# Kernel optimization log

Measured on AMD Instinct MI355X. Metric: run time of the kernel, lower is better.

The kernel has to match this reference:

```python
import jax, jax.numpy as jnp
import numpy as np

# Static config (matches init_kwargs)
B = 1; Z = 64; H = 64; W = 64; C = 96
NH = 3; WS = 4; SS = 2
N = WS ** 3                      # tokens per 3D window = 64
NW = (Z // WS) * (H // WS) * (W // WS)   # num windows = 4096
SCALE = (C // NH) ** -0.5
EPS = 1e-5


def _rel_pos_index():
    # same construction as WindowAttention3D.__init__ (torch.meshgrid default 'ij')
    coords = np.stack(np.meshgrid(np.arange(WS), np.arange(WS), np.arange(WS), indexing='ij'))
    cf = coords.reshape(3, -1)                       # (3, N)
    rc = (cf[:, :, None] - cf[:, None, :]).transpose(1, 2, 0)  # (N, N, 3)
    rc[:, :, 0] += WS - 1; rc[:, :, 1] += WS - 1; rc[:, :, 2] += WS - 1
    rc[:, :, 0] *= (2 * WS - 1) ** 2
    rc[:, :, 1] *= (2 * WS - 1)
    return rc.sum(-1)                                # (N, N) int


def _attn_mask():
    # shifted-window mask, as in SwinTransformerBlock3D.__init__
    img = np.zeros((Z, H, W), dtype=np.float32)
    sl = (slice(0, -WS), slice(-WS, -SS), slice(-SS, None))
    cnt = 0
    for z in sl:
        for h in sl:
            for w in sl:
                img[z, h, w] = cnt
                cnt += 1
    mw = img.reshape(Z // WS, WS, H // WS, WS, W // WS, WS)
    mw = mw.transpose(0, 2, 4, 1, 3, 5).reshape(-1, N)        # (nW, N)
    am = mw[:, None, :] - mw[:, :, None]                      # (nW, N, N)
    return np.where(am != 0, np.float32(-100.0), np.float32(0.0))


REL_IDX = jnp.asarray(_rel_pos_index())        # (N, N) int32, closed-over constant
ATTN_MASK = jnp.asarray(_attn_mask())          # (nW, N, N) float32


def _layernorm(x, g, b):
    m = x.mean(-1, keepdims=True)
    v = ((x - m) ** 2).mean(-1, keepdims=True)
    return (x - m) * jax.lax.rsqrt(v + EPS) * g + b


def _window_partition(x):
    # (B, Z, H, W, C) -> (B*nW, N, C)
    x = x.reshape(B, Z // WS, WS, H // WS, WS, W // WS, WS, C)
    return x.transpose(0, 1, 3, 5, 2, 4, 6, 7).reshape(-1, N, C)


def _window_reverse(wins):
    # (B*nW, N, C) -> (B, Z, H, W, C)
    x = wins.reshape(B, Z // WS, H // WS, W // WS, WS, WS, WS, C)
    return x.transpose(0, 1, 4, 2, 5, 3, 6, 7).reshape(B, Z, H, W, C)


def setup_inputs() -> dict:
    key = jax.random.key(0)
    ks = jax.random.split(key, 8)
    d = {
        'x': jax.random.normal(ks[0], (B, Z * H * W, C), jnp.float32),
        'norm1_w': jnp.ones((C,), jnp.float32),
        'norm1_b': jnp.zeros((C,), jnp.float32),
        'qkv_w': jax.random.normal(ks[1], (3 * C, C), jnp.float32) * 0.02,
        'qkv_b': jnp.zeros((3 * C,), jnp.float32),
        'rel_bias': jax.random.normal(ks[2], ((2 * WS - 1) ** 3, NH), jnp.float32) * 0.02,
        'proj_w': jax.random.normal(ks[3], (C, C), jnp.float32) * 0.02,
        'proj_b': jnp.zeros((C,), jnp.float32),
        'norm2_w': jnp.ones((C,), jnp.float32),
        'norm2_b': jnp.zeros((C,), jnp.float32),
        'fc1_w': jax.random.normal(ks[4], (4 * C, C), jnp.float32) * 0.02,
        'fc1_b': jnp.zeros((4 * C,), jnp.float32),
        'fc2_w': jax.random.normal(ks[5], (C, 4 * C), jnp.float32) * 0.02,
        'fc2_b': jnp.zeros((C,), jnp.float32),
    }
    return d


def reference(x, norm1_w, norm1_b, qkv_w, qkv_b, rel_bias, proj_w, proj_b,
              norm2_w, norm2_b, fc1_w, fc1_b, fc2_w, fc2_b):
    shortcut = x
    h = _layernorm(x, norm1_w, norm1_b).reshape(B, Z, H, W, C)
    # cyclic shift (SW-MSA)
    h = jnp.roll(h, (-SS, -SS, -SS), axis=(1, 2, 3))
    xw = _window_partition(h)                                  # (B*nW, N, C)
    qkv = (xw @ qkv_w.T + qkv_b).reshape(-1, N, 3, NH, C // NH)
    qkv = qkv.transpose(2, 0, 3, 1, 4)                         # (3, B_, NH, N, hd)
    q, k, v = qkv[0] * SCALE, qkv[1], qkv[2]
    attn = jnp.einsum('bhnd,bhmd->bhnm', q, k)                 # (B_, NH, N, N)
    bias = rel_bias[REL_IDX.reshape(-1)].reshape(N, N, NH).transpose(2, 0, 1)
    attn = attn + bias[None]
    attn = attn.reshape(B, NW, NH, N, N) + ATTN_MASK[None, :, None]
    attn = jax.nn.softmax(attn.reshape(-1, NH, N, N), axis=-1)
    out = jnp.einsum('bhnm,bhmd->bhnd', attn, v)
    out = out.transpose(0, 2, 1, 3).reshape(-1, N, C)
    out = out @ proj_w.T + proj_b
    h = _window_reverse(out)
    h = jnp.roll(h, (SS, SS, SS), axis=(1, 2, 3)).reshape(B, Z * H * W, C)
    x = shortcut + h                                            # residual (drop_path=0)
    y = _layernorm(x, norm2_w, norm2_b)
    y = jax.nn.gelu(y @ fc1_w.T + fc1_b, approximate=False)
    y = y @ fc2_w.T + fc2_b
    return x + y
```

## Files before the change

kernel.cpp:

```cpp
#include <hip/hip_runtime.h>

typedef __attribute__((ext_vector_type(8))) short short8;
typedef __attribute__((ext_vector_type(4))) float f32x4;

static __device__ __forceinline__ unsigned short f2bf(float f) {
  return (unsigned short)((__builtin_bit_cast(unsigned int, f) + 0x8000u) >> 16);
}
static __device__ __forceinline__ float bf2f(unsigned short u) {
  return __builtin_bit_cast(float, ((unsigned)u) << 16);
}
static __device__ __forceinline__ unsigned cvtpk(float a, float b) {
  unsigned r;
  asm("v_cvt_pk_bf16_f32 %0, %1, %2" : "=v"(r) : "v"(a), "v"(b));
  return r;
}

constexpr float LOG2E = 1.4426950408889634f;
constexpr float QSCL = 0.17677669529663687f * LOG2E;
constexpr int XP = 104;
constexpr int KP = 104;
constexpr int VTP = 72;

static __device__ __forceinline__ int frag_src(int o, int K) {
  const int j = o & 7;
  const int lane = (o >> 3) & 63;
  const int f = o >> 9;
  const int nks = K >> 5;
  const int ks = f % nks;
  const int t = f / nks;
  const int row = t * 16 + (lane & 15);
  const int k = ks * 32 + (lane >> 4) * 8 + j;
  return row * K + k;
}

__global__ void prep_kernel(const float* __restrict__ qkvw, const float* __restrict__ projw,
                            const float* __restrict__ fc1w, const float* __restrict__ fc2w,
                            const float* __restrict__ relbias,
                            unsigned short* __restrict__ ws, float* __restrict__ tab) {
  int i = blockIdx.x * 256 + threadIdx.x;
  if (i < 27648) ws[i] = f2bf(qkvw[frag_src(i, 96)] * (i < 9216 ? QSCL : 1.f));
  if (i < 9216)  ws[27648 + i] = f2bf(projw[frag_src(i, 96)]);
  if (i < 36864) {
    ws[36864 + i] = f2bf(fc1w[frag_src(i, 96)]);
    ws[73728 + i] = f2bf(fc2w[frag_src(i, 384)]);
  }
  if (i < 98304) {
    const int r = i & 3, kgi = (i >> 2) & 3, q = (i >> 4) & 63, nt = (i >> 10) & 3;
    const int vh = i >> 12;
    const int h = vh % 3, v = vh / 3;
    const int key = nt * 16 + kgi * 4 + r;
    const bool bz = v & 4, bh = v & 2, bw = v & 1;
    const int iz = q >> 4, ih = (q >> 2) & 3, iw = q & 3;
    const int jz = key >> 4, jh = (key >> 2) & 3, jw = key & 3;
    const int idx = (iz - jz + 3) * 49 + (ih - jh + 3) * 7 + (iw - jw + 3);
    const int ci = (bz ? (iz < 2 ? 9 : 18) : 0) + (bh ? (ih < 2 ? 3 : 6) : 0) +
                   (bw ? (iw < 2 ? 1 : 2) : 0);
    const int cj = (bz ? (jz < 2 ? 9 : 18) : 0) + (bh ? (jh < 2 ? 3 : 6) : 0) +
                   (bw ? (jw < 2 ? 1 : 2) : 0);
    tab[i] = (relbias[idx * 3 + h] + (ci != cj ? -100.f : 0.f)) * LOG2E;
  }
}

__global__ __launch_bounds__(256, 4) void fused_kernel(
    const float* __restrict__ x,
    const float* __restrict__ n1w, const float* __restrict__ n1b,
    const float* __restrict__ qkvb, const float* __restrict__ tab,
    const float* __restrict__ projb,
    const float* __restrict__ n2w, const float* __restrict__ n2b,
    const float* __restrict__ b1, const float* __restrict__ b2,
    const unsigned short* __restrict__ wq, const unsigned short* __restrict__ wp,
    const unsigned short* __restrict__ w1, const unsigned short* __restrict__ w2,
    float* __restrict__ out) {
  __shared__ unsigned short Xo[64 * XP];
  __shared__ unsigned short Kb[64 * KP];
  __shared__ unsigned short Vt[96 * VTP];

  const int tid = threadIdx.x;
  const int bid = blockIdx.x;
  const int wz = bid >> 8, wh = (bid >> 4) & 15, ww = bid & 15;
  const int wave = tid >> 6, lane = tid & 63;
  const int ln = lane & 15, kg = lane >> 4;

  {
    const int n = tid >> 2, part = tid & 3;
    const int lz = n >> 4, lh = (n >> 2) & 3, lw = n & 3;
    const int sz = (wz * 4 + lz + 2) & 63;
    const int sh = (wh * 4 + lh + 2) & 63;
    const int sw = (ww * 4 + lw + 2) & 63;
    const float* px = x + (size_t)((sz * 64 + sh) * 64 + sw) * 96 + part * 24;
    float4 v[6];
#pragma unroll
    for (int j = 0; j < 6; ++j) v[j] = ((const float4*)px)[j];
    float s = 0.f, sq = 0.f;
#pragma unroll
    for (int j = 0; j < 6; ++j) {
      s += v[j].x + v[j].y + v[j].z + v[j].w;
      sq += v[j].x * v[j].x + v[j].y * v[j].y + v[j].z * v[j].z + v[j].w * v[j].w;
    }
    s += __shfl_xor(s, 1);  s += __shfl_xor(s, 2);
    sq += __shfl_xor(sq, 1); sq += __shfl_xor(sq, 2);
    const float mean = s * (1.f / 96.f);
    const float var = sq * (1.f / 96.f) - mean * mean;
    const float rs = rsqrtf(var + 1e-5f);
    const float4* g4 = (const float4*)(n1w + part * 24);
    const float4* b4 = (const float4*)(n1b + part * 24);
#pragma unroll
    for (int j = 0; j < 6; ++j) {
      float4 g = g4[j], b = b4[j];
      uint2 o;
      o.x = cvtpk((v[j].x - mean) * rs * g.x + b.x, (v[j].y - mean) * rs * g.y + b.y);
      o.y = cvtpk((v[j].z - mean) * rs * g.z + b.z, (v[j].w - mean) * rs * g.w + b.w);
      *(uint2*)&Xo[n * XP + part * 24 + j * 4] = o;
    }
  }

  short8 qa[3];
  {
    short8 a[3];
#pragma unroll
    for (int ks = 0; ks < 3; ++ks)
      a[ks] = *(const short8*)&Xo[(wave * 16 + ln) * XP + ks * 32 + kg * 8];
#pragma unroll
    for (int g = 0; g < 3; ++g) {
      short8 wf[6];
#pragma unroll
      for (int f = 0; f < 6; ++f)
        wf[f] = *(const short8*)&wq[(size_t)(g * 6 + f) * 512 + lane * 8];
#pragma unroll
      for (int t = 0; t < 2; ++t) {
        const int nt = g * 2 + t;
        const int oc = nt * 16 + ln;
        f32x4 acc = {0.f, 0.f, 0.f, 0.f};
#pragma unroll
        for (int ks = 0; ks < 3; ++ks)
          acc = __builtin_amdgcn_mfma_f32_16x16x32_bf16(a[ks], wf[t * 3 + ks], acc, 0, 0, 0);
        const float bias = qkvb[oc];
#pragma unroll
        for (int r = 0; r < 4; ++r)
          Kb[(wave * 16 + kg * 4 + r) * KP + oc] = f2bf(fmaf(bias, QSCL, acc[r]));
      }
    }
#pragma unroll
    for (int h = 0; h < 3; ++h)
      qa[h] = *(const short8*)&Kb[(wave * 16 + ln) * KP + h * 32 + kg * 8];
  }
  __syncthreads();

  {
    const int t0 = wave < 2 ? 6 + 2 * wave : 8 + wave;
    const int t1 = wave < 2 ? 7 + 2 * wave : 10 + 2 * wave;
    const int t2 = wave < 2 ? 12 + wave : 11 + 2 * wave;
#pragma unroll
    for (int i = 0; i < 3; ++i) {
      const int tile = i == 0 ? t0 : (i == 1 ? t1 : t2);
      const int oc = tile * 16 + ln;
      short8 wf[3];
#pragma unroll
      for (int ks = 0; ks < 3; ++ks)
        wf[ks] = *(const short8*)&wq[(size_t)(tile * 3 + ks) * 512 + lane * 8];
      const float bias = qkvb[oc];
#pragma unroll
      for (int rt = 0; rt < 4; ++rt) {
        f32x4 acc = {0.f, 0.f, 0.f, 0.f};
#pragma unroll
        for (int ks = 0; ks < 3; ++ks) {
          short8 a = *(const short8*)&Xo[(rt * 16 + ln) * XP + ks * 32 + kg * 8];
          acc = __builtin_amdgcn_mfma_f32_16x16x32_bf16(a, wf[ks], acc, 0, 0, 0);
        }
        if (tile < 12) {
#pragma unroll
          for (int r = 0; r < 4; ++r)
            Kb[(rt * 16 + kg * 4 + r) * KP + (tile - 12 + 6) * 16 + ln] = f2bf(acc[r] + bias);
        } else {
          uint2 u;
          u.x = cvtpk(acc[0] + bias, acc[1] + bias);
          u.y = cvtpk(acc[2] + bias, acc[3] + bias);
          *(uint2*)&Vt[((tile - 12) * 16 + ln) * VTP + rt * 16 + kg * 4] = u;
        }
      }
    }
  }
  __syncthreads();

  const int vv = ((wz == 15) ? 4 : 0) | ((wh == 15) ? 2 : 0) | ((ww == 15) ? 1 : 0);
  const float* tb0 = tab + (size_t)(vv * 3) * 4096;
  const int rowbase = wave * 16 + kg * 4;
  const int lA = ((kg & 1) << 5) + ln;
  const int lB = lA + 16;
#pragma unroll
  for (int h = 0; h < 3; ++h) {
    const float* tb = tb0 + h * 4096;
    f32x4 e[4];
#pragma unroll
    for (int nt = 0; nt < 4; ++nt) {
      short8 kf = *(const short8*)&Kb[(nt * 16 + ln) * KP + h * 32 + kg * 8];
      f32x4 trow = *(const f32x4*)(tb + nt * 1024 + (wave * 16 + ln) * 16 + kg * 4);
      f32x4 z = {0.f, 0.f, 0.f, 0.f};
      f32x4 st = __builtin_amdgcn_mfma_f32_16x16x32_bf16(kf, qa[h], z, 0, 0, 0);
#pragma unroll
      for (int r = 0; r < 4; ++r)
        e[nt][r] = __builtin_amdgcn_exp2f(st[r] + trow[r]);
    }
    float hs = 0.f;
#pragma unroll
    for (int nt = 0; nt < 4; ++nt)
#pragma unroll
      for (int r = 0; r < 4; ++r) hs += e[nt][r];
    hs += __shfl_xor(hs, 16);
    hs += __shfl_xor(hs, 32);
    const float inv = __builtin_amdgcn_rcpf(hs);
    unsigned pp[4][2];
#pragma unroll
    for (int nt = 0; nt < 4; ++nt) {
      pp[nt][0] = cvtpk(e[nt][0] * inv, e[nt][1] * inv);
      pp[nt][1] = cvtpk(e[nt][2] * inv, e[nt][3] * inv);
    }
    short8 paf[2];
#pragma unroll
    for (int ks = 0; ks < 2; ++ks) {
      const unsigned a0 = __shfl((int)pp[2 * ks][0], lA);
      const unsigned a1 = __shfl((int)pp[2 * ks][1], lA);
      const unsigned a2 = __shfl((int)pp[2 * ks][0], lB);
      const unsigned a3 = __shfl((int)pp[2 * ks][1], lB);
      const unsigned b0 = __shfl((int)pp[2 * ks + 1][0], lA);
      const unsigned b1 = __shfl((int)pp[2 * ks + 1][1], lA);
      const unsigned b2 = __shfl((int)pp[2 * ks + 1][0], lB);
      const unsigned b3 = __shfl((int)pp[2 * ks + 1][1], lB);
      const bool hi = (kg >> 1) != 0;
      uint4 wv;
      wv.x = hi ? b0 : a0;
      wv.y = hi ? b1 : a1;
      wv.z = hi ? b2 : a2;
      wv.w = hi ? b3 : a3;
      paf[ks] = __builtin_bit_cast(short8, wv);
    }
#pragma unroll
    for (int dt = 0; dt < 2; ++dt) {
      f32x4 oacc = {0.f, 0.f, 0.f, 0.f};
#pragma unroll
      for (int ks = 0; ks < 2; ++ks) {
        short8 vb = *(const short8*)&Vt[(h * 32 + dt * 16 + ln) * VTP + ks * 32 + kg * 8];
        oacc = __builtin_amdgcn_mfma_f32_16x16x32_bf16(paf[ks], vb, oacc, 0, 0, 0);
      }
#pragma unroll
      for (int r = 0; r < 4; ++r)
        Xo[(rowbase + r) * XP + h * 32 + dt * 16 + ln] = f2bf(oacc[r]);
    }
  }
  __syncthreads();

  unsigned short* X2b = Vt;

  {
    int gtok[4];
#pragma unroll
    for (int r = 0; r < 4; ++r) {
      const int n = rowbase + r;
      const int lz = n >> 4, lh = (n >> 2) & 3, lw = n & 3;
      const int oz = (wz * 4 + lz + 2) & 63;
      const int oh = (wh * 4 + lh + 2) & 63;
      const int ow = (ww * 4 + lw + 2) & 63;
      gtok[r] = (oz * 64 + oh) * 64 + ow;
    }
    short8 oa[3];
#pragma unroll
    for (int ks = 0; ks < 3; ++ks)
      oa[ks] = *(const short8*)&Xo[(wave * 16 + ln) * XP + ks * 32 + kg * 8];
    float s_[4] = {0.f, 0.f, 0.f, 0.f}, sq_[4] = {0.f, 0.f, 0.f, 0.f};
#pragma unroll
    for (int g = 0; g < 3; ++g) {
      short8 wf[6];
#pragma unroll
      for (int f = 0; f < 6; ++f)
        wf[f] = *(const short8*)&wp[(size_t)(g * 6 + f) * 512 + lane * 8];
#pragma unroll
      for (int t = 0; t < 2; ++t) {
        const int nt = g * 2 + t;
        const int col = nt * 16 + ln;
        f32x4 acc = {0.f, 0.f, 0.f, 0.f};
#pragma unroll
        for (int ks = 0; ks < 3; ++ks)
          acc = __builtin_amdgcn_mfma_f32_16x16x32_bf16(oa[ks], wf[t * 3 + ks], acc, 0, 0, 0);
        const float pbv = projb[col];
#pragma unroll
        for (int r = 0; r < 4; ++r) {
          const float v = x[(size_t)gtok[r] * 96 + col] + acc[r] + pbv;
          s_[r] += v;
          sq_[r] += v * v;
          X2b[(rowbase + r) * XP + col] = f2bf(v);
        }
      }
    }
#pragma unroll
    for (int r = 0; r < 4; ++r) {
      float s = s_[r], sq = sq_[r];
      s += __shfl_xor(s, 1);  s += __shfl_xor(s, 2);
      s += __shfl_xor(s, 4);  s += __shfl_xor(s, 8);
      sq += __shfl_xor(sq, 1); sq += __shfl_xor(sq, 2);
      sq += __shfl_xor(sq, 4); sq += __shfl_xor(sq, 8);
      const float mean = s * (1.f / 96.f);
      const float var = sq * (1.f / 96.f) - mean * mean;
      const float rs = rsqrtf(var + 1e-5f);
      s_[r] = mean;
      sq_[r] = rs;
    }
#pragma unroll
    for (int nt = 0; nt < 6; ++nt) {
      const int col = nt * 16 + ln;
      const float gw = n2w[col], gb = n2b[col];
#pragma unroll
      for (int r = 0; r < 4; ++r) {
        const float v = bf2f(X2b[(rowbase + r) * XP + col]);
        const float xl = (v - s_[r]) * sq_[r] * gw + gb;
        Xo[(rowbase + r) * XP + col] = f2bf(xl);
      }
    }
  }

  const int nf1 = (wave < 2) ? 1 : 2;
  const int f1base = (wave < 2) ? wave : 2 + 2 * (wave - 2);
  const int nf2 = (wave < 2) ? 2 : 1;
  const int f2base = (wave < 2) ? 2 * wave : 2 + wave;
  f32x4 acc2[2][4];
#pragma unroll
  for (int i = 0; i < 2; ++i)
#pragma unroll
    for (int rt = 0; rt < 4; ++rt) acc2[i][rt] = (f32x4){0.f, 0.f, 0.f, 0.f};

#pragma unroll 1
  for (int c = 0; c < 4; ++c) {
    __syncthreads();
#pragma unroll
    for (int i = 0; i < 2; ++i) {
      if (i < nf1) {
        const int tile = f1base + i;
        short8 wf1[3];
#pragma unroll
        for (int ks = 0; ks < 3; ++ks)
          wf1[ks] = *(const short8*)&w1[(size_t)(c * 18 + tile * 3 + ks) * 512 + lane * 8];
        const float bb = b1[c * 96 + tile * 16 + ln];
#pragma unroll
        for (int rt = 0; rt < 4; ++rt) {
          f32x4 acc = {0.f, 0.f, 0.f, 0.f};
#pragma unroll
          for (int ks = 0; ks < 3; ++ks) {
            short8 a = *(const short8*)&Xo[(rt * 16 + ln) * XP + ks * 32 + kg * 8];
            acc = __builtin_amdgcn_mfma_f32_16x16x32_bf16(a, wf1[ks], acc, 0, 0, 0);
          }
#pragma unroll
          for (int r = 0; r < 4; ++r) {
            const float v = acc[r] + bb;
            const float t2 = v * v;
            float p = fmaf(0.004287f, t2, -0.05694f);
            p = fmaf(p, t2, 0.3952f);
            float phi = fmaf(p, v, 0.5f);
            phi = fminf(fmaxf(phi, 0.f), 1.f);
            Kb[(rt * 16 + kg * 4 + r) * KP + tile * 16 + ln] = f2bf(v * phi);
          }
        }
      }
    }
    __syncthreads();
#pragma unroll
    for (int ks = 0; ks < 3; ++ks) {
      short8 wf2[2];
#pragma unroll
      for (int i = 0; i < 2; ++i)
        if (i < nf2)
          wf2[i] = *(const short8*)&w2[(size_t)((f2base + i) * 12 + c * 3 + ks) * 512 + lane * 8];
#pragma unroll
      for (int rt = 0; rt < 4; ++rt) {
        short8 pa = *(const short8*)&Kb[(rt * 16 + ln) * KP + ks * 32 + kg * 8];
#pragma unroll
        for (int i = 0; i < 2; ++i)
          if (i < nf2)
            acc2[i][rt] = __builtin_amdgcn_mfma_f32_16x16x32_bf16(pa, wf2[i], acc2[i][rt], 0, 0, 0);
      }
    }
  }

#pragma unroll
  for (int i = 0; i < 2; ++i) {
    if (i < nf2) {
      const int col = (f2base + i) * 16 + ln;
      const float bb = b2[col];
#pragma unroll
      for (int rt = 0; rt < 4; ++rt) {
#pragma unroll
        for (int r = 0; r < 4; ++r) {
          const int n = rt * 16 + kg * 4 + r;
          const int lz = n >> 4, lh = (n >> 2) & 3, lw = n & 3;
          const int oz = (wz * 4 + lz + 2) & 63;
          const int oh = (wh * 4 + lh + 2) & 63;
          const int ow = (ww * 4 + lw + 2) & 63;
          const size_t gt = (size_t)((oz * 64 + oh) * 64 + ow);
          const float v = bf2f(X2b[n * XP + col]);
          out[gt * 96 + col] = v + acc2[i][rt][r] + bb;
        }
      }
    }
  }
}

extern "C" void kernel_launch(void* const* d_in, const int* in_sizes, int n_in,
                              void* d_out, int out_size, void* d_ws, size_t ws_size,
                              hipStream_t stream) {
  const float* x    = (const float*)d_in[0];
  const float* n1w  = (const float*)d_in[1];
  const float* n1b  = (const float*)d_in[2];
  const float* qkvw = (const float*)d_in[3];
  const float* qkvb = (const float*)d_in[4];
  const float* relb = (const float*)d_in[5];
  const float* pw   = (const float*)d_in[6];
  const float* pb   = (const float*)d_in[7];
  const float* n2w  = (const float*)d_in[8];
  const float* n2b  = (const float*)d_in[9];
  const float* w1   = (const float*)d_in[10];
  const float* b1   = (const float*)d_in[11];
  const float* w2   = (const float*)d_in[12];
  const float* b2   = (const float*)d_in[13];
  float* out = (float*)d_out;

  unsigned short* wsq = (unsigned short*)d_ws;
  unsigned short* wsp = wsq + 27648;
  unsigned short* ws1 = wsp + 9216;
  unsigned short* ws2 = ws1 + 36864;
  float* tab = (float*)(wsq + 110592);

  hipLaunchKernelGGL(prep_kernel, dim3(384), dim3(256), 0, stream,
                     qkvw, pw, w1, w2, relb, wsq, tab);
  hipLaunchKernelGGL(fused_kernel, dim3(4096), dim3(256), 0, stream,
                     x, n1w, n1b, qkvb, tab, pb, n2w, n2b, b1, b2,
                     wsq, wsp, ws1, ws2, out);
}
```

Before: 140.1 us.

## Process two adjacent windows per 512-thread block to share weight fragments

Each block now handles two neighbouring windows along W with 8 waves and double-sized shared buffers. The K/V projection and MLP stages are redistributed so each wave loads a weight fragment once and applies it to both windows, which cuts global weight-fragment loads per window and balances the tile work across waves. The cost is double the LDS per block, which lowers how many blocks fit per CU, and the 512-thread launch bound with a min-blocks hint of 4 may raise register pressure.

New measurement: 155.2 us. 1.11x slower.

```diff
diff --git a/kernel.cpp b/kernel.cpp
--- a/kernel.cpp
+++ b/kernel.cpp
@@ -61,7 +61,7 @@
   }
 }
 
-__global__ __launch_bounds__(256, 4) void fused_kernel(
+__global__ __launch_bounds__(512, 4) void fused_kernel(
     const float* __restrict__ x,
     const float* __restrict__ n1w, const float* __restrict__ n1b,
     const float* __restrict__ qkvb, const float* __restrict__ tab,
@@ -71,22 +71,24 @@
     const unsigned short* __restrict__ wq, const unsigned short* __restrict__ wp,
     const unsigned short* __restrict__ w1, const unsigned short* __restrict__ w2,
     float* __restrict__ out) {
-  __shared__ unsigned short Xo[64 * XP];
-  __shared__ unsigned short Kb[64 * KP];
-  __shared__ unsigned short Vt[96 * VTP];
+  __shared__ unsigned short Xo[2][64 * XP];
+  __shared__ unsigned short Kb[2][64 * KP];
+  __shared__ unsigned short Vt[2][96 * VTP];
 
   const int tid = threadIdx.x;
   const int bid = blockIdx.x;
-  const int wz = bid >> 8, wh = (bid >> 4) & 15, ww = bid & 15;
+  const int wz = bid >> 7, wh = (bid >> 3) & 15, wwbase = (bid << 1) & 15;
   const int wave = tid >> 6, lane = tid & 63;
   const int ln = lane & 15, kg = lane >> 4;
+  const int win = wave >> 2, wv = wave & 3;
+  const int ww_w = wwbase + win;
 
   {
-    const int n = tid >> 2, part = tid & 3;
+    const int n = (tid >> 2) & 63, wt = tid >> 8, part = tid & 3;
     const int lz = n >> 4, lh = (n >> 2) & 3, lw = n & 3;
     const int sz = (wz * 4 + lz + 2) & 63;
     const int sh = (wh * 4 + lh + 2) & 63;
-    const int sw = (ww * 4 + lw + 2) & 63;
+    const int sw = ((wwbase + wt) * 4 + lw + 2) & 63;
     const float* px = x + (size_t)((sz * 64 + sh) * 64 + sw) * 96 + part * 24;
     float4 v[6];
 #pragma unroll
@@ -110,7 +112,7 @@
       uint2 o;
       o.x = cvtpk((v[j].x - mean) * rs * g.x + b.x, (v[j].y - mean) * rs * g.y + b.y);
       o.y = cvtpk((v[j].z - mean) * rs * g.z + b.z, (v[j].w - mean) * rs * g.w + b.w);
-      *(uint2*)&Xo[n * XP + part * 24 + j * 4] = o;
+      *(uint2*)&Xo[wt][n * XP + part * 24 + j * 4] = o;
     }
   }
 
@@ -119,7 +121,7 @@
     short8 a[3];
 #pragma unroll
     for (int ks = 0; ks < 3; ++ks)
-      a[ks] = *(const short8*)&Xo[(wave * 16 + ln) * XP + ks * 32 + kg * 8];
+      a[ks] = *(const short8*)&Xo[win][(wv * 16 + ln) * XP + ks * 32 + kg * 8];
 #pragma unroll
     for (int g = 0; g < 3; ++g) {
       short8 wf[6];
@@ -137,64 +139,68 @@
         const float bias = qkvb[oc];
 #pragma unroll
         for (int r = 0; r < 4; ++r)
-          Kb[(wave * 16 + kg * 4 + r) * KP + oc] = f2bf(fmaf(bias, QSCL, acc[r]));
+          Kb[win][(wv * 16 + kg * 4 + r) * KP + oc] = f2bf(fmaf(bias, QSCL, acc[r]));
       }
     }
 #pragma unroll
     for (int h = 0; h < 3; ++h)
-      qa[h] = *(const short8*)&Kb[(wave * 16 + ln) * KP + h * 32 + kg * 8];
+      qa[h] = *(const short8*)&Kb[win][(wv * 16 + ln) * KP + h * 32 + kg * 8];
   }
   __syncthreads();
 
   {
-    const int t0 = wave < 2 ? 6 + 2 * wave : 8 + wave;
-    const int t1 = wave < 2 ? 7 + 2 * wave : 10 + 2 * wave;
-    const int t2 = wave < 2 ? 12 + wave : 11 + 2 * wave;
-#pragma unroll
-    for (int i = 0; i < 3; ++i) {
-      const int tile = i == 0 ? t0 : (i == 1 ? t1 : t2);
-      const int oc = tile * 16 + ln;
-      short8 wf[3];
-#pragma unroll
-      for (int ks = 0; ks < 3; ++ks)
-        wf[ks] = *(const short8*)&wq[(size_t)(tile * 3 + ks) * 512 + lane * 8];
-      const float bias = qkvb[oc];
+    const int ta = (3 * wave) >> 1;
+    const int tb = ta + 1;
+    const int odd = wave & 1;
+    short8 wfa[3], wfb[3];
+#pragma unroll
+    for (int ks = 0; ks < 3; ++ks) {
+      wfa[ks] = *(const short8*)&wq[(size_t)((6 + ta) * 3 + ks) * 512 + lane * 8];
+      wfb[ks] = *(const short8*)&wq[(size_t)((6 + tb) * 3 + ks) * 512 + lane * 8];
+    }
+#pragma unroll
+    for (int j = 0; j < 3; ++j) {
+      const int wj = (j == 1) ? (odd ^ 1) : odd;
+      const int tj = (j == 0) ? ta : ((j == 2) ? tb : (odd ? tb : ta));
+      const bool useB = (tj != ta);
+      const float bias = qkvb[96 + tj * 16 + ln];
 #pragma unroll
       for (int rt = 0; rt < 4; ++rt) {
         f32x4 acc = {0.f, 0.f, 0.f, 0.f};
 #pragma unroll
         for (int ks = 0; ks < 3; ++ks) {
-          short8 a = *(const short8*)&Xo[(rt * 16 + ln) * XP + ks * 32 + kg * 8];
-          acc = __builtin_amdgcn_mfma_f32_16x16x32_bf16(a, wf[ks], acc, 0, 0, 0);
-        }
-        if (tile < 12) {
+          short8 a = *(const short8*)&Xo[wj][(rt * 16 + ln) * XP + ks * 32 + kg * 8];
+          acc = __builtin_amdgcn_mfma_f32_16x16x32_bf16(
+              a, useB ? wfb[ks] : wfa[ks], acc, 0, 0, 0);
+        }
+        if (tj < 6) {
 #pragma unroll
           for (int r = 0; r < 4; ++r)
-            Kb[(rt * 16 + kg * 4 + r) * KP + (tile - 12 + 6) * 16 + ln] = f2bf(acc[r] + bias);
+            Kb[wj][(rt * 16 + kg * 4 + r) * KP + tj * 16 + ln] = f2bf(acc[r] + bias);
         } else {
           uint2 u;
           u.x = cvtpk(acc[0] + bias, acc[1] + bias);
           u.y = cvtpk(acc[2] + bias, acc[3] + bias);
-          *(uint2*)&Vt[((tile - 12) * 16 + ln) * VTP + rt * 16 + kg * 4] = u;
+          *(uint2*)&Vt[wj][((tj - 6) * 16 + ln) * VTP + rt * 16 + kg * 4] = u;
         }
       }
     }
   }
   __syncthreads();
 
-  const int vv = ((wz == 15) ? 4 : 0) | ((wh == 15) ? 2 : 0) | ((ww == 15) ? 1 : 0);
+  const int vv = ((wz == 15) ? 4 : 0) | ((wh == 15) ? 2 : 0) | ((ww_w == 15) ? 1 : 0);
   const float* tb0 = tab + (size_t)(vv * 3) * 4096;
-  const int rowbase = wave * 16 + kg * 4;
+  const int rowbase = wv * 16 + kg * 4;
   const int lA = ((kg & 1) << 5) + ln;
   const int lB = lA + 16;
 #pragma unroll
   for (int h = 0; h < 3; ++h) {
-    const float* tb = tb0 + h * 4096;
+    const float* tbh = tb0 + h * 4096;
     f32x4 e[4];
 #pragma unroll
     for (int nt = 0; nt < 4; ++nt) {
-      short8 kf = *(const short8*)&Kb[(nt * 16 + ln) * KP + h * 32 + kg * 8];
-      f32x4 trow = *(const f32x4*)(tb + nt * 1024 + (wave * 16 + ln) * 16 + kg * 4);
+      short8 kf = *(const short8*)&Kb[win][(nt * 16 + ln) * KP + h * 32 + kg * 8];
+      f32x4 trow = *(const f32x4*)(tbh + nt * 1024 + (wv * 16 + ln) * 16 + kg * 4);
       f32x4 z = {0.f, 0.f, 0.f, 0.f};
       f32x4 st = __builtin_amdgcn_mfma_f32_16x16x32_bf16(kf, qa[h], z, 0, 0, 0);
 #pragma unroll
@@ -227,31 +233,30 @@
       const unsigned b2 = __shfl((int)pp[2 * ks + 1][0], lB);
       const unsigned b3 = __shfl((int)pp[2 * ks + 1][1], lB);
       const bool hi = (kg >> 1) != 0;
-      uint4 wv;
-      wv.x = hi ? b0 : a0;
-      wv.y = hi ? b1 : a1;
-      wv.z = hi ? b2 : a2;
-      wv.w = hi ? b3 : a3;
-      paf[ks] = __builtin_bit_cast(short8, wv);
+      uint4 wvv;
+      wvv.x = hi ? b0 : a0;
+      wvv.y = hi ? b1 : a1;
+      wvv.z = hi ? b2 : a2;
+      wvv.w = hi ? b3 : a3;
+      paf[ks] = __builtin_bit_cast(short8, wvv);
     }
 #pragma unroll
     for (int dt = 0; dt < 2; ++dt) {
       f32x4 oacc = {0.f, 0.f, 0.f, 0.f};
 #pragma unroll
       for (int ks = 0; ks < 2; ++ks) {
-        short8 vb = *(const short8*)&Vt[(h * 32 + dt * 16 + ln) * VTP + ks * 32 + kg * 8];
+        short8 vb = *(const short8*)&Vt[win][(h * 32 + dt * 16 + ln) * VTP + ks * 32 + kg * 8];
         oacc = __builtin_amdgcn_mfma_f32_16x16x32_bf16(paf[ks], vb, oacc, 0, 0, 0);
       }
 #pragma unroll
       for (int r = 0; r < 4; ++r)
-        Xo[(rowbase + r) * XP + h * 32 + dt * 16 + ln] = f2bf(oacc[r]);
+        Xo[win][(rowbase + r) * XP + h * 32 + dt * 16 + ln] = f2bf(oacc[r]);
     }
   }
   __syncthreads();
 
-  unsigned short* X2b = Vt;
-
   {
+    unsigned short* X2w = &Vt[win][0];
     int gtok[4];
 #pragma unroll
     for (int r = 0; r < 4; ++r) {
@@ -259,13 +264,13 @@
       const int lz = n >> 4, lh = (n >> 2) & 3, lw = n & 3;
       const int oz = (wz * 4 + lz + 2) & 63;
       const int oh = (wh * 4 + lh + 2) & 63;
-      const int ow = (ww * 4 + lw + 2) & 63;
+      const int ow = (ww_w * 4 + lw + 2) & 63;
       gtok[r] = (oz * 64 + oh) * 64 + ow;
     }
     short8 oa[3];
 #pragma unroll
     for (int ks = 0; ks < 3; ++ks)
-      oa[ks] = *(const short8*)&Xo[(wave * 16 + ln) * XP + ks * 32 + kg * 8];
+      oa[ks] = *(const short8*)&Xo[win][(wv * 16 + ln) * XP + ks * 32 + kg * 8];
     float s_[4] = {0.f, 0.f, 0.f, 0.f}, sq_[4] = {0.f, 0.f, 0.f, 0.f};
 #pragma unroll
     for (int g = 0; g < 3; ++g) {
@@ -287,7 +292,7 @@
           const float v = x[(size_t)gtok[r] * 96 + col] + acc[r] + pbv;
           s_[r] += v;
           sq_[r] += v * v;
-          X2b[(rowbase + r) * XP + col] = f2bf(v);
+          X2w[(rowbase + r) * XP + col] = f2bf(v);
         }
       }
     }
@@ -310,17 +315,19 @@
       const float gw = n2w[col], gb = n2b[col];
 #pragma unroll
       for (int r = 0; r < 4; ++r) {
-        const float v = bf2f(X2b[(rowbase + r) * XP + col]);
+        const float v = bf2f(X2w[(rowbase + r) * XP + col]);
         const float xl = (v - s_[r]) * sq_[r] * gw + gb;
-        Xo[(rowbase + r) * XP + col] = f2bf(xl);
-      }
-    }
-  }
-
-  const int nf1 = (wave < 2) ? 1 : 2;
-  const int f1base = (wave < 2) ? wave : 2 + 2 * (wave - 2);
-  const int nf2 = (wave < 2) ? 2 : 1;
-  const int f2base = (wave < 2) ? 2 * wave : 2 + wave;
+        Xo[win][(rowbase + r) * XP + col] = f2bf(xl);
+      }
+    }
+  }
+
+  const int nW1 = (wave < 4) ? 1 : 2;
+  const int f1t = (wave < 4) ? (wave >> 1) : (wave - 2);
+  const int f1w0 = (wave < 4) ? (wave & 1) : 0;
+  const int nW2 = (wave < 4) ? 2 : 1;
+  const int f2t = (wave < 4) ? wave : 4 + ((wave - 4) >> 1);
+  const int f2w0 = (wave < 4) ? 0 : ((wave - 4) & 1);
   f32x4 acc2[2][4];
 #pragma unroll
   for (int i = 0; i < 2; ++i)
@@ -330,71 +337,75 @@
 #pragma unroll 1
   for (int c = 0; c < 4; ++c) {
     __syncthreads();
-#pragma unroll
-    for (int i = 0; i < 2; ++i) {
-      if (i < nf1) {
-        const int tile = f1base + i;
-        short8 wf1[3];
-#pragma unroll
-        for (int ks = 0; ks < 3; ++ks)
-          wf1[ks] = *(const short8*)&w1[(size_t)(c * 18 + tile * 3 + ks) * 512 + lane * 8];
-        const float bb = b1[c * 96 + tile * 16 + ln];
-#pragma unroll
-        for (int rt = 0; rt < 4; ++rt) {
-          f32x4 acc = {0.f, 0.f, 0.f, 0.f};
-#pragma unroll
-          for (int ks = 0; ks < 3; ++ks) {
-            short8 a = *(const short8*)&Xo[(rt * 16 + ln) * XP + ks * 32 + kg * 8];
-            acc = __builtin_amdgcn_mfma_f32_16x16x32_bf16(a, wf1[ks], acc, 0, 0, 0);
+    {
+      short8 wf1[3];
+#pragma unroll
+      for (int ks = 0; ks < 3; ++ks)
+        wf1[ks] = *(const short8*)&w1[(size_t)(c * 18 + f1t * 3 + ks) * 512 + lane * 8];
+      const float bb = b1[c * 96 + f1t * 16 + ln];
+#pragma unroll
+      for (int i = 0; i < 2; ++i) {
+        if (i < nW1) {
+          const int win1 = f1w0 + i;
+#pragma unroll
+          for (int rt = 0; rt < 4; ++rt) {
+            f32x4 acc = {0.f, 0.f, 0.f, 0.f};
+#pragma unroll
+            for (int ks = 0; ks < 3; ++ks) {
+              short8 a = *(const short8*)&Xo[win1][(rt * 16 + ln) * XP + ks * 32 + kg * 8];
+              acc = __builtin_amdgcn_mfma_f32_16x16x32_bf16(a, wf1[ks], acc, 0, 0, 0);
+            }
+#pragma unroll
+            for (int r = 0; r < 4; ++r) {
+              const float v = acc[r] + bb;
+              const float t2 = v * v;
+              float p = fmaf(0.004287f, t2, -0.05694f);
+              p = fmaf(p, t2, 0.3952f);
+              float phi = fmaf(p, v, 0.5f);
+              phi = fminf(fmaxf(phi, 0.f), 1.f);
+              Kb[win1][(rt * 16 + kg * 4 + r) * KP + f1t * 16 + ln] = f2bf(v * phi);
+            }
           }
-#pragma unroll
-          for (int r = 0; r < 4; ++r) {
-            const float v = acc[r] + bb;
-            const float t2 = v * v;
-            float p = fmaf(0.004287f, t2, -0.05694f);
-            p = fmaf(p, t2, 0.3952f);
-            float phi = fmaf(p, v, 0.5f);
-            phi = fminf(fmaxf(phi, 0.f), 1.f);
-            Kb[(rt * 16 + kg * 4 + r) * KP + tile * 16 + ln] = f2bf(v * phi);
+        }
+      }
+    }
+    __syncthreads();
+#pragma unroll
+    for (int ks = 0; ks < 3; ++ks) {
+      short8 wf2 = *(const short8*)&w2[(size_t)(f2t * 12 + c * 3 + ks) * 512 + lane * 8];
+#pragma unroll
+      for (int i = 0; i < 2; ++i) {
+        if (i < nW2) {
+          const int win2 = f2w0 + i;
+#pragma unroll
+          for (int rt = 0; rt < 4; ++rt) {
+            short8 pa = *(const short8*)&Kb[win2][(rt * 16 + ln) * KP + ks * 32 + kg * 8];
+            acc2[i][rt] = __builtin_amdgcn_mfma_f32_16x16x32_bf16(pa, wf2, acc2[i][rt], 0, 0, 0);
           }
         }
       }
     }
-    __syncthreads();
-#pragma unroll
-    for (int ks = 0; ks < 3; ++ks) {
-      short8 wf2[2];
-#pragma unroll
-      for (int i = 0; i < 2; ++i)
-        if (i < nf2)
-          wf2[i] = *(const short8*)&w2[(size_t)((f2base + i) * 12 + c * 3 + ks) * 512 + lane * 8];
-#pragma unroll
-      for (int rt = 0; rt < 4; ++rt) {
-        short8 pa = *(const short8*)&Kb[(rt * 16 + ln) * KP + ks * 32 + kg * 8];
-#pragma unroll
-        for (int i = 0; i < 2; ++i)
-          if (i < nf2)
-            acc2[i][rt] = __builtin_amdgcn_mfma_f32_16x16x32_bf16(pa, wf2[i], acc2[i][rt], 0, 0, 0);
-      }
-    }
   }
 
 #pragma unroll
   for (int i = 0; i < 2; ++i) {
-    if (i < nf2) {
-      const int col = (f2base + i) * 16 + ln;
+    if (i < nW2) {
+      const int win2 = f2w0 + i;
+      const int col = f2t * 16 + ln;
       const float bb = b2[col];
+      const unsigned short* X2w = &Vt[win2][0];
+      const int wwc = wwbase + win2;
 #pragma unroll
       for (int rt = 0; rt < 4; ++rt) {
 #pragma unroll
         for (int r = 0; r < 4; ++r) {
           const int n = rt * 16 + kg * 4 + r;
-          const int lz = n >> 4, lh = (n >> 2) & 3, lw = n & 3;
-          const int oz = (wz * 4 + lz + 2) & 63;
+          const int lh = (n >> 2) & 3, lw = n & 3;
+          const int oz = (wz * 4 + rt + 2) & 63;
           const int oh = (wh * 4 + lh + 2) & 63;
-          const int ow = (ww * 4 + lw + 2) & 63;
+          const int ow = (wwc * 4 + lw + 2) & 63;
           const size_t gt = (size_t)((oz * 64 + oh) * 64 + ow);
-          const float v = bf2f(X2b[n * XP + col]);
+          const float v = bf2f(X2w[n * XP + col]);
           out[gt * 96 + col] = v + acc2[i][rt][r] + bb;
         }
       }
@@ -429,7 +440,7 @@
 
   hipLaunchKernelGGL(prep_kernel, dim3(384), dim3(256), 0, stream,
                      qkvw, pw, w1, w2, relb, wsq, tab);
-  hipLaunchKernelGGL(fused_kernel, dim3(4096), dim3(256), 0, stream,
+  hipLaunchKernelGGL(fused_kernel, dim3(2048), dim3(512), 0, stream,
                      x, n1w, n1b, qkvb, tab, pb, n2w, n2b, b1, b2,
                      wsq, wsp, ws1, ws2, out);
 }
```
